# Performance work log

Hardware: AMD Instinct MI355X
Metric: run time of the kernel (lower is better)

Reference implementation:

```python
import jax, jax.numpy as jnp
import numpy as np

N = 100000   # nodes
E = 1600000  # edges
IN_DIM = 64
OUT_DIM = 64
HEADS = 4
C = OUT_DIM // HEADS  # per-head channels = 16
EDGE_DIM = 16
NEG_SLOPE = 0.2
EPS = 1e-5


def setup_inputs() -> dict:
    key = jax.random.key(0)
    ks = jax.random.split(key, 16)
    s = 0.1
    return {
        "x": jax.random.normal(ks[0], (N, IN_DIM), jnp.float32),
        "edge_index": jax.random.randint(ks[1], (2, E), 0, N, jnp.int64 if jax.config.jax_enable_x64 else jnp.int32),
        "edge_attr": jax.random.normal(ks[2], (E, EDGE_DIM), jnp.float32),
        # GATv2Conv params (share_weights=False, edge_dim, concat=True)
        "Wl": jax.random.normal(ks[3], (IN_DIM, HEADS * C), jnp.float32) * s,
        "bl": jnp.zeros((HEADS * C,), jnp.float32),
        "Wr": jax.random.normal(ks[4], (IN_DIM, HEADS * C), jnp.float32) * s,
        "br": jnp.zeros((HEADS * C,), jnp.float32),
        "We": jax.random.normal(ks[5], (EDGE_DIM, HEADS * C), jnp.float32) * s,
        "att": jax.random.normal(ks[6], (HEADS, C), jnp.float32) * s,
        "conv_bias": jnp.zeros((HEADS * C,), jnp.float32),
        # edge gate MLP: Linear(edge_dim, 2*edge_dim) -> SiLU -> Linear(2*edge_dim, 1) -> Sigmoid
        "Wg1": jax.random.normal(ks[7], (EDGE_DIM, 2 * EDGE_DIM), jnp.float32) * s,
        "bg1": jnp.zeros((2 * EDGE_DIM,), jnp.float32),
        "Wg2": jax.random.normal(ks[8], (2 * EDGE_DIM, 1), jnp.float32) * s,
        "bg2": jnp.zeros((1,), jnp.float32),
        # LayerNorm(out_dim)
        "gamma": jnp.ones((OUT_DIM,), jnp.float32),
        "beta": jnp.zeros((OUT_DIM,), jnp.float32),
    }


def _silu(v):
    return v * jax.nn.sigmoid(v)


def reference(x, edge_index, edge_attr, Wl, bl, Wr, br, We, att, conv_bias,
              Wg1, bg1, Wg2, bg2, gamma, beta):
    src, tgt = edge_index[0], edge_index[1]

    # --- edge gate: sigmoid(Linear(SiLU(Linear(e)))) -> [E, 1]
    gate = jax.nn.sigmoid(_silu(edge_attr @ Wg1 + bg1) @ Wg2 + bg2)

    # --- GATv2Conv ---
    xl = (x @ Wl + bl).reshape(N, HEADS, C)   # source transform
    xr = (x @ Wr + br).reshape(N, HEADS, C)   # target transform
    ee = (edge_attr @ We).reshape(E, HEADS, C)

    xj = xl[src]                               # [E, H, C] source messages
    m = jax.nn.leaky_relu(xj + xr[tgt] + ee, NEG_SLOPE)
    alpha = jnp.einsum('ehc,hc->eh', m, att)   # [E, H]

    # segment softmax over edges sharing the same target node
    amax = jax.ops.segment_max(alpha, tgt, num_segments=N)  # [N, H]
    a = jnp.exp(alpha - amax[tgt])
    denom = jax.ops.segment_sum(a, tgt, num_segments=N)
    a = a / denom[tgt]

    out = jax.ops.segment_sum(xj * a[:, :, None], tgt, num_segments=N)
    out = out.reshape(N, HEADS * C) + conv_bias

    # --- edge-gate mean modulation per target node ---
    gate_sum = jax.ops.segment_sum(gate[:, 0], tgt, num_segments=N)
    degree = jax.ops.segment_sum(jnp.ones((E,), out.dtype), tgt, num_segments=N)
    mean_gate = gate_sum / jnp.maximum(degree, 1.0)
    out = out * mean_gate[:, None]

    # --- LayerNorm -> SiLU -> (dropout p=0) -> residual (Identity proj) ---
    mu = jnp.mean(out, axis=-1, keepdims=True)
    var = jnp.var(out, axis=-1, keepdims=True)
    out = (out - mu) * jax.lax.rsqrt(var + EPS) * gamma + beta
    out = _silu(out)
    return out + x
```

## Files before the change

### kernel.cpp

```cpp
#include <hip/hip_runtime.h>
#include <hip/hip_bf16.h>
#include <hip/hip_fp16.h>
#include <math.h>

#define N_NODES 100000
#define N_EDGES 1600000
#define IN_DIM 64
#define OUT_DIM 64
#define HEADS 4
#define CH 16
#define EDGE_DIM 16
#define NEG_SLOPE 0.2f
#define LN_EPS 1e-5f
#define NBLK 391
#define CHUNK 32
#define NREP 8

typedef unsigned short u16;
typedef unsigned int u32;
typedef unsigned long long u64;
typedef __attribute__((ext_vector_type(8))) short bf16x8;
typedef __attribute__((ext_vector_type(4))) float f32x4;

__device__ __forceinline__ float bf2f(u16 v) {
    return __uint_as_float(((u32)v) << 16);
}
__device__ __forceinline__ u16 f2bf(float f) {
    u32 u = __float_as_uint(f);
    u32 r = (u + 0x7FFFu + ((u >> 16) & 1u)) >> 16;
    return (u16)r;
}
__device__ __forceinline__ void load16bf(const u16* p, float* out) {
    const uint4* q = (const uint4*)p;
    uint4 a = q[0], b = q[1];
    u32 w[8] = {a.x, a.y, a.z, a.w, b.x, b.y, b.z, b.w};
#pragma unroll
    for (int i = 0; i < 8; ++i) {
        out[2*i]   = __uint_as_float(w[i] << 16);
        out[2*i+1] = __uint_as_float(w[i] & 0xFFFF0000u);
    }
}
__device__ __forceinline__ void load16f(const void* base, long i, bool f32in, float* out) {
    if (f32in) {
        const float4* q = (const float4*)((const float*)base + i);
        float4 v0 = q[0], v1 = q[1], v2 = q[2], v3 = q[3];
        out[0]=v0.x; out[1]=v0.y; out[2]=v0.z; out[3]=v0.w;
        out[4]=v1.x; out[5]=v1.y; out[6]=v1.z; out[7]=v1.w;
        out[8]=v2.x; out[9]=v2.y; out[10]=v2.z; out[11]=v2.w;
        out[12]=v3.x; out[13]=v3.y; out[14]=v3.z; out[15]=v3.w;
    } else {
        load16bf((const u16*)base + i, out);
    }
}
__device__ __forceinline__ float ldf(const void* base, int i, bool f32in) {
    return f32in ? ((const float*)base)[i] : bf2f(((const u16*)base)[i]);
}

#define DPP_ROR_ADD(v, N) do { \
    int _d = __builtin_amdgcn_update_dpp(0, __float_as_int(v), 0x120 + (N), 0xF, 0xF, true); \
    (v) += __int_as_float(_d); } while (0)

__global__ void k_sniff_zero(const u32* __restrict__ xw, const int* __restrict__ eiw,
                             int* __restrict__ flags, int4* __restrict__ curR4,
                             float4* __restrict__ gsum4) {
    if (blockIdx.x != 0) {
        const int i = (blockIdx.x - 1) * 256 + threadIdx.x;
        if (i < NREP * N_NODES / 4) curR4[i] = make_int4(0, 0, 0, 0);
        else if (i < NREP * N_NODES / 4 + N_NODES / 4)
            gsum4[i - NREP * N_NODES / 4] = make_float4(0.f, 0.f, 0.f, 0.f);
        return;
    }
    __shared__ int s_f32, s_not64;
    const int t = threadIdx.x;
    if (t == 0) { s_f32 = 0; s_not64 = 0; }
    __syncthreads();
    if (t < 64) {
        u32 w = xw[t];
        for (int h = 0; h < 2; ++h) {
            u32 bits = h ? (w & 0xFFFF0000u) : (w << 16);
            float v = __uint_as_float(bits);
            float a = fabsf(v);
            bool sane = (a == 0.0f) || (a >= 1e-30f && a <= 1000.0f);
            if (!sane || v != v) atomicOr(&s_f32, 1);
        }
    } else if (t < 96) {
        if (eiw[2 * (t - 64) + 1] != 0) atomicOr(&s_not64, 1);
    }
    __syncthreads();
    if (t == 0) flags[0] = s_f32 | ((s_not64 ? 0 : 1) << 1);
}

__global__ __launch_bounds__(256) void k_transform(
    const void* __restrict__ x,
    const void* __restrict__ Wl, const void* __restrict__ bl,
    const void* __restrict__ Wr, const void* __restrict__ br,
    u16* __restrict__ xl, u16* __restrict__ xr,
    const int* __restrict__ flags)
{
    const bool f32in = (flags[0] & 1) != 0;
    const int lane = threadIdx.x & 63;
    const int w = threadIdx.x >> 6;
    const int m0 = blockIdx.x * 64;
    const int col = lane & 15;
    const int quad = lane >> 4;

    bf16x8 bfrag[2][2];
    float bias[2];
#pragma unroll
    for (int nt = 0; nt < 2; ++nt) {
        const int ng = w * 32 + nt * 16 + col;
        const void* W  = (ng < 64) ? Wl : Wr;
        const void* bi = (ng < 64) ? bl : br;
        const int c = ng & 63;
        bias[nt] = ldf(bi, c, f32in);
#pragma unroll
        for (int kf = 0; kf < 2; ++kf)
#pragma unroll
            for (int j = 0; j < 8; ++j) {
                const int k = kf * 32 + quad * 8 + j;
                bfrag[nt][kf][j] = (short)f2bf(ldf(W, k * 64 + c, f32in));
            }
    }

#pragma unroll
    for (int mt = 0; mt < 4; ++mt) {
        const int mrow = m0 + mt * 16 + col;
        const int m = (mrow < N_NODES) ? mrow : (N_NODES - 1);
        bf16x8 afrag[2];
#pragma unroll
        for (int kf = 0; kf < 2; ++kf) {
            const int kb = kf * 32 + quad * 8;
            if (f32in) {
                const float* xp = (const float*)x + (size_t)m * 64 + kb;
#pragma unroll
                for (int j = 0; j < 8; ++j) afrag[kf][j] = (short)f2bf(xp[j]);
            } else {
                afrag[kf] = *(const bf16x8*)((const u16*)x + (size_t)m * 64 + kb);
            }
        }
#pragma unroll
        for (int nt = 0; nt < 2; ++nt) {
            f32x4 c = {bias[nt], bias[nt], bias[nt], bias[nt]};
            c = __builtin_amdgcn_mfma_f32_16x16x32_bf16(afrag[0], bfrag[nt][0], c, 0, 0, 0);
            c = __builtin_amdgcn_mfma_f32_16x16x32_bf16(afrag[1], bfrag[nt][1], c, 0, 0, 0);
            const int ng = w * 32 + nt * 16 + col;
            u16* dst = (ng < 64) ? xl : xr;
            const int cc = ng & 63;
#pragma unroll
            for (int r = 0; r < 4; ++r) {
                const int node = m0 + mt * 16 + quad * 4 + r;
                if (node < N_NODES) dst[(size_t)node * 64 + cc] = f2bf(c[r]);
            }
        }
    }
}

__global__ __launch_bounds__(256) void k_count_gate(
    const int* __restrict__ ei, int* __restrict__ curR,
    float4* __restrict__ zreg, u16* __restrict__ slotA, u16* __restrict__ gateA,
    const void* __restrict__ edge_attr,
    const void* __restrict__ Wg1, const void* __restrict__ bg1,
    const void* __restrict__ Wg2, const void* __restrict__ bg2,
    const int* __restrict__ flags)
{
    __shared__ float sWg1t[32 * 16];
    __shared__ float sBg1[32];
    __shared__ float sWg2[32];
    __shared__ float sBg2;
    const int tid = threadIdx.x;
    const int fl = flags[0];
    const bool f32in = (fl & 1) != 0;
    const bool i64   = (fl & 2) != 0;
    for (int i = tid; i < 32 * 16; i += 256) {
        const int j = i >> 4, k = i & 15;
        sWg1t[i] = ldf(Wg1, k * 32 + j, f32in);
    }
    if (tid < 32) sBg1[tid] = ldf(bg1, tid, f32in);
    if (tid >= 32 && tid < 64) sWg2[tid - 32] = ldf(Wg2, tid - 32, f32in);
    if (tid == 0) sBg2 = ldf(bg2, 0, f32in);
    __syncthreads();

    const int gid = blockIdx.x * 256 + tid;
    for (int i = gid; i < N_NODES * 68 / 4; i += 6250 * 256)
        zreg[i] = make_float4(0.f, 0.f, 0.f, 0.f);
    const int tgt = i64 ? ei[2 * (N_EDGES + gid)] : ei[N_EDGES + gid];
    const int r = blockIdx.x & (NREP - 1);
    const int slot = atomicAdd(&curR[r * N_NODES + tgt], 1);
    slotA[gid] = (u16)slot;

    float ea[EDGE_DIM];
    load16f(edge_attr, (long)gid * EDGE_DIM, f32in, ea);
    float g = sBg2;
#pragma unroll
    for (int j = 0; j < 32; ++j) {
        float hv = sBg1[j];
        const float4* wr = (const float4*)&sWg1t[j * 16];
#pragma unroll
        for (int k4 = 0; k4 < 4; ++k4) {
            const float4 wv = wr[k4];
            hv += ea[4*k4]   * wv.x + ea[4*k4+1] * wv.y
                + ea[4*k4+2] * wv.z + ea[4*k4+3] * wv.w;
        }
        hv = hv / (1.f + __expf(-hv));
        g += hv * sWg2[j];
    }
    g = 1.f / (1.f + __expf(-g));
    gateA[gid] = __half_as_ushort(__float2half(g));
}

__global__ __launch_bounds__(256) void k_bsum(const int* __restrict__ curR,
                                              int* __restrict__ partial)
{
    const int i = blockIdx.x * 256 + threadIdx.x;
    int v = 0;
    if (i < N_NODES) {
#pragma unroll
        for (int r = 0; r < NREP; ++r) v += curR[r * N_NODES + i];
    }
#pragma unroll
    for (int off = 32; off >= 1; off >>= 1) v += __shfl_xor(v, off, 64);
    __shared__ int ws[4];
    if ((threadIdx.x & 63) == 0) ws[threadIdx.x >> 6] = v;
    __syncthreads();
    if (threadIdx.x == 0) partial[blockIdx.x] = ws[0] + ws[1] + ws[2] + ws[3];
}

__global__ void k_bscan(const int* __restrict__ partial, int* __restrict__ poff,
                        int* __restrict__ base)
{
    __shared__ int sp[NBLK];
    for (int i = threadIdx.x; i < NBLK; i += 64) sp[i] = partial[i];
    __syncthreads();
    if (threadIdx.x == 0) {
        int run = 0;
        for (int i = 0; i < NBLK; ++i) { int t = sp[i]; sp[i] = run; run += t; }
        base[N_NODES] = N_EDGES;
    }
    __syncthreads();
    for (int i = threadIdx.x; i < NBLK; i += 64) poff[i] = sp[i];
}

__global__ __launch_bounds__(256) void k_bfinal(int* __restrict__ curR,
                                                const int* __restrict__ poff,
                                                int* __restrict__ base)
{
    const int i = blockIdx.x * 256 + threadIdx.x;
    const int lane = threadIdx.x & 63;
    const int wave = threadIdx.x >> 6;
    int c[NREP];
    int v = 0;
    if (i < N_NODES) {
#pragma unroll
        for (int r = 0; r < NREP; ++r) { c[r] = curR[r * N_NODES + i]; v += c[r]; }
    }
    int s = v;
#pragma unroll
    for (int off = 1; off < 64; off <<= 1) {
        int t = __shfl_up(s, off, 64);
        if (lane >= off) s += t;
    }
    __shared__ int wsum[4];
    if (lane == 63) wsum[wave] = s;
    __syncthreads();
    int wb = 0;
    for (int w = 0; w < wave; ++w) wb += wsum[w];
    if (i < N_NODES) {
        int run = poff[blockIdx.x] + wb + s - v;
        base[i] = run;
#pragma unroll
        for (int r = 0; r < NREP; ++r) { curR[r * N_NODES + i] = run; run += c[r]; }
    }
}

__global__ __launch_bounds__(256) void k_scatter(
    const int* __restrict__ ei, const int* __restrict__ curR,
    const u16* __restrict__ slotA,
    u64* __restrict__ perm8, const int* __restrict__ flags)
{
    const int e = blockIdx.x * 256 + threadIdx.x;
    const bool i64 = (flags[0] & 2) != 0;
    int src, tgt;
    if (i64) { src = ei[2 * e]; tgt = ei[2 * (N_EDGES + e)]; }
    else     { src = ei[e];     tgt = ei[N_EDGES + e]; }
    const int r = blockIdx.x & (NREP - 1);
    const int pos = curR[r * N_NODES + tgt] + (int)slotA[e];
    perm8[pos] = (u64)(u32)src | ((u64)(u32)tgt << 17) | ((u64)(u32)e << 34);
}


__device__ __forceinline__ void seg_flush(
    float* __restrict__ accum, float* __restrict__ dsum_g, float* __restrict__ gsum,
    int t, int lane, float acc, float dsum, float gs)
{
    atomicAdd(&accum[(size_t)t * 64 + lane], acc);
    if ((lane & 15) == 0) atomicAdd(&dsum_g[t * 4 + (lane >> 4)], dsum);
    if (lane == 1) atomicAdd(&gsum[t], gs);
}

template<bool F32IN>
__device__ __forceinline__ void ea_issue(const void* __restrict__ edge_attr,
                                         int eid, uint4* r)
{
    if constexpr (F32IN) {
        const uint4* q = (const uint4*)edge_attr + (size_t)eid * 4;
        r[0] = q[0]; r[1] = q[1]; r[2] = q[2]; r[3] = q[3];
    } else {
        const uint4* q = (const uint4*)((const u16*)edge_attr + (size_t)eid * 16);
        r[0] = q[0]; r[1] = q[1];
    }
}

template<bool F32IN>
__device__ __forceinline__ void ea_vals(const uint4* r, float* out)
{
    const u32* w = (const u32*)r;
    if constexpr (F32IN) {
#pragma unroll
        for (int i = 0; i < 16; ++i) out[i] = __uint_as_float(w[i]);
    } else {
#pragma unroll
        for (int i = 0; i < 8; ++i) {
            out[2*i]   = __uint_as_float(w[i] << 16);
            out[2*i+1] = __uint_as_float(w[i] & 0xFFFF0000u);
        }
    }
}

#define PERM_EXTRACT(JJ, S, T, E2) do { \
    const u32 _lo = (u32)__builtin_amdgcn_readlane(plo, (JJ)); \
    const u32 _hi = (u32)__builtin_amdgcn_readlane(phi, (JJ)); \
    (S)  = (int)(_lo & 0x1FFFFu); \
    (T)  = (int)(((_lo >> 17) | (_hi << 15)) & 0x1FFFFu); \
    (E2) = (int)(_hi >> 2); } while (0)

template<bool F32IN>
__device__ __forceinline__ void attn_run(
    const u64* __restrict__ perm8, const void* __restrict__ edge_attr,
    const u16* __restrict__ gateA,
    const u16* __restrict__ xl, const u16* __restrict__ xr,
    float* __restrict__ accum, float* __restrict__ dsum_g, float* __restrict__ gsum,
    const float* We_c, float att_c, int lane, int j0)
{
    const u64 pl = perm8[j0 + (lane & (CHUNK - 1))];
    const int plo = (int)(u32)pl;
    const int phi = (int)(u32)(pl >> 32);

    int s_cur, t_cur, e_cur;
    PERM_EXTRACT(0, s_cur, t_cur, e_cur);

    uint4 ear[F32IN ? 4 : 2];
    ea_issue<F32IN>(edge_attr, e_cur, ear);
    u32 xl_c = xl[(size_t)s_cur * 64 + lane];
    u32 xr_c = xr[(size_t)t_cur * 64 + lane];
    float g_c = __half2float(__ushort_as_half(gateA[e_cur]));

    int cur_t = t_cur;
    float acc = 0.f, dsum = 0.f, gs = 0.f;

#pragma unroll
    for (int jj = 0; jj < CHUNK; ++jj) {
        float eav[16];
        ea_vals<F32IN>(ear, eav);
        float ee = 0.f;
#pragma unroll
        for (int k = 0; k < EDGE_DIM; ++k) ee = fmaf(eav[k], We_c[k], ee);
        const float xlf = bf2f((u16)xl_c);
        const float xrf = bf2f((u16)xr_c);

        int s_nxt = s_cur, t_nxt = t_cur, e_nxt = e_cur;
        u32 xl_n = xl_c, xr_n = xr_c;
        float g_n = g_c;
        if (jj + 1 < CHUNK) {
            PERM_EXTRACT(jj + 1, s_nxt, t_nxt, e_nxt);
            ea_issue<F32IN>(edge_attr, e_nxt, ear);
            xl_n = xl[(size_t)s_nxt * 64 + lane];
            g_n = __half2float(__ushort_as_half(gateA[e_nxt]));
            if (t_nxt != t_cur)
                xr_n = xr[(size_t)t_nxt * 64 + lane];
        }

        if (t_cur != cur_t) {
            seg_flush(accum, dsum_g, gsum, cur_t, lane, acc, dsum, gs);
            cur_t = t_cur; acc = 0.f; dsum = 0.f; gs = 0.f;
        }
        float m = xlf + xrf + ee;
        m = fmaxf(m, m * NEG_SLOPE);
        float t = att_c * m;
        DPP_ROR_ADD(t, 1);
        DPP_ROR_ADD(t, 2);
        DPP_ROR_ADD(t, 4);
        DPP_ROR_ADD(t, 8);
        const float a = __expf(t);
        acc  += a * xlf;
        dsum += a;
        gs   += g_c;

        s_cur = s_nxt; t_cur = t_nxt; e_cur = e_nxt;
        xl_c = xl_n;   xr_c = xr_n;   g_c = g_n;
    }
    seg_flush(accum, dsum_g, gsum, cur_t, lane, acc, dsum, gs);
}

__global__ __launch_bounds__(256, 8) void k_attn_agg(
    const u64* __restrict__ perm8,
    const void* __restrict__ edge_attr,
    const u16* __restrict__ gateA,
    const void* __restrict__ We,
    const void* __restrict__ att,
    const u16* __restrict__ xl, const u16* __restrict__ xr,
    float* __restrict__ accum,
    float* __restrict__ dsum_g,
    float* __restrict__ gsum,
    const int* __restrict__ flags)
{
    const bool f32in = (flags[0] & 1) != 0;
    const int lane = threadIdx.x & 63;
    const int wid = blockIdx.x * 4 + (threadIdx.x >> 6);
    const int j0 = wid * CHUNK;

    float We_c[EDGE_DIM];
#pragma unroll
    for (int k = 0; k < EDGE_DIM; ++k) We_c[k] = ldf(We, k * 64 + lane, f32in);
    const float att_c = ldf(att, lane, f32in);

    if (f32in) attn_run<true >(perm8, edge_attr, gateA, xl, xr, accum, dsum_g, gsum, We_c, att_c, lane, j0);
    else       attn_run<false>(perm8, edge_attr, gateA, xl, xr, accum, dsum_g, gsum, We_c, att_c, lane, j0);
}

__global__ __launch_bounds__(256) void k_epilogue(
    const int* __restrict__ base,
    const float* __restrict__ accum, const float* __restrict__ dsum_g,
    const float* __restrict__ gsum,
    const void* __restrict__ conv_bias, const void* __restrict__ gamma,
    const void* __restrict__ beta, const void* __restrict__ x,
    void* __restrict__ out, const int* __restrict__ flags)
{
    const bool f32in = (flags[0] & 1) != 0;
    const int lane = threadIdx.x & 63;
    const int wave = threadIdx.x >> 6;
    const int n = blockIdx.x * 4 + wave;
    if (n >= N_NODES) return;
    const int h = lane >> 4;

    float v = accum[(size_t)n * 64 + lane];
    const float d = dsum_g[n * 4 + h];
    v = (d > 0.f) ? v / d : 0.f;
    v += ldf(conv_bias, lane, f32in);
    const int deg = base[n + 1] - base[n];
    const float mg = gsum[n] / fmaxf((float)deg, 1.0f);
    v *= mg;

    float s = v;
#pragma unroll
    for (int m2 = 32; m2 >= 1; m2 >>= 1) s += __shfl_xor(s, m2, 64);
    const float mu = s * (1.f / 64.f);
    const float diff = v - mu;
    float q = diff * diff;
#pragma unroll
    for (int m2 = 32; m2 >= 1; m2 >>= 1) q += __shfl_xor(q, m2, 64);
    const float var = q * (1.f / 64.f);

    float y = diff * rsqrtf(var + LN_EPS) * ldf(gamma, lane, f32in) + ldf(beta, lane, f32in);
    y = y / (1.f + __expf(-y));
    const float r = y + ldf(x, n * 64 + lane, f32in);
    if (f32in) ((float*)out)[(size_t)n * 64 + lane] = r;
    else       ((u16*)out)[(size_t)n * 64 + lane] = f2bf(r);
}

extern "C" void kernel_launch(void* const* d_in, const int* in_sizes, int n_in,
                              void* d_out, int out_size, void* d_ws, size_t ws_size,
                              hipStream_t stream)
{
    const void* x   = d_in[0];
    const int* ei   = (const int*)d_in[1];
    const void* ea  = d_in[2];
    const void* Wl  = d_in[3];
    const void* bl  = d_in[4];
    const void* Wr  = d_in[5];
    const void* br  = d_in[6];
    const void* We  = d_in[7];
    const void* att = d_in[8];
    const void* cb  = d_in[9];
    const void* Wg1 = d_in[10];
    const void* bg1 = d_in[11];
    const void* Wg2 = d_in[12];
    const void* bg2 = d_in[13];
    const void* gam = d_in[14];
    const void* bet = d_in[15];

    char* ws = (char*)d_ws;
    int*   flags   = (int*)ws;
    int*   curR    = (int*)(ws + 16);
    int*   base    = (int*)(ws + 3200016);
    int*   partial = (int*)(ws + 3600032);
    int*   poff    = (int*)(ws + 3601600);
    u16*   slotA   = (u16*)(ws + 3603168);
    u16*   gateA   = (u16*)(ws + 6803168);
    u64*   perm8   = (u64*)(ws + 10003168);
    float* accum   = (float*)(ws + 22803168);
    float* dsum_g  = (float*)(ws + 48403168);
    float* gsum    = (float*)(ws + 50003168);
    u16*   xl      = (u16*)(ws + 50403168);
    u16*   xr      = (u16*)(ws + 63203168);

    k_sniff_zero<<<881, 256, 0, stream>>>((const u32*)x, ei, flags, (int4*)curR,
                                          (float4*)gsum);

    k_transform<<<(N_NODES + 63) / 64, 256, 0, stream>>>(x, Wl, bl, Wr, br, xl, xr, flags);

    k_count_gate<<<N_EDGES / 256, 256, 0, stream>>>(
        ei, curR, (float4*)accum, slotA, gateA, ea, Wg1, bg1, Wg2, bg2, flags);

    k_bsum<<<NBLK, 256, 0, stream>>>(curR, partial);
    k_bscan<<<1, 64, 0, stream>>>(partial, poff, base);
    k_bfinal<<<NBLK, 256, 0, stream>>>(curR, poff, base);

    k_scatter<<<N_EDGES / 256, 256, 0, stream>>>(ei, curR, slotA, perm8, flags);

    k_attn_agg<<<N_EDGES / CHUNK / 4, 256, 0, stream>>>(
        perm8, ea, gateA, We, att, xl, xr, accum, dsum_g, gsum, flags);

    k_epilogue<<<(N_NODES + 3) / 4, 256, 0, stream>>>(
        base, accum, dsum_g, gsum, cb, gam, bet, x, d_out, flags);
}
```

Before: 468.2 us.

## Accumulate edge gates per target in count kernel; double-buffer edge_attr loads

The per-edge gate is no longer written to a half-precision array and re-read in the attention kernel. The count kernel now atomically adds it into replicated per-target sums (8 replicas), and the epilogue reduces those with shuffles. The attention loop double-buffers edge_attr prefetches and uses packed 2-wide FMAs for the edge projection. This removes a per-edge gather and a per-segment atomic from the hot attention kernel, at the cost of extra float atomics in the count kernel and a larger zeroing pass.

```diff
diff --git a/kernel.cpp b/kernel.cpp
--- a/kernel.cpp
+++ b/kernel.cpp
@@ -21,6 +21,7 @@
 typedef unsigned long long u64;
 typedef __attribute__((ext_vector_type(8))) short bf16x8;
 typedef __attribute__((ext_vector_type(4))) float f32x4;
+typedef __attribute__((ext_vector_type(2))) float f32x2;
 
 __device__ __forceinline__ float bf2f(u16 v) {
     return __uint_as_float(((u32)v) << 16);
@@ -62,12 +63,12 @@
 
 __global__ void k_sniff_zero(const u32* __restrict__ xw, const int* __restrict__ eiw,
                              int* __restrict__ flags, int4* __restrict__ curR4,
-                             float4* __restrict__ gsum4) {
+                             float4* __restrict__ gsumR4) {
     if (blockIdx.x != 0) {
         const int i = (blockIdx.x - 1) * 256 + threadIdx.x;
         if (i < NREP * N_NODES / 4) curR4[i] = make_int4(0, 0, 0, 0);
-        else if (i < NREP * N_NODES / 4 + N_NODES / 4)
-            gsum4[i - NREP * N_NODES / 4] = make_float4(0.f, 0.f, 0.f, 0.f);
+        else if (i < 2 * NREP * N_NODES / 4)
+            gsumR4[i - NREP * N_NODES / 4] = make_float4(0.f, 0.f, 0.f, 0.f);
         return;
     }
     __shared__ int s_f32, s_not64;
@@ -157,7 +158,7 @@
 
 __global__ __launch_bounds__(256) void k_count_gate(
     const int* __restrict__ ei, int* __restrict__ curR,
-    float4* __restrict__ zreg, u16* __restrict__ slotA, u16* __restrict__ gateA,
+    float4* __restrict__ zreg, u16* __restrict__ slotA, float* __restrict__ gsumR,
     const void* __restrict__ edge_attr,
     const void* __restrict__ Wg1, const void* __restrict__ bg1,
     const void* __restrict__ Wg2, const void* __restrict__ bg2,
@@ -190,6 +191,7 @@
 
     float ea[EDGE_DIM];
     load16f(edge_attr, (long)gid * EDGE_DIM, f32in, ea);
+
     float g = sBg2;
 #pragma unroll
     for (int j = 0; j < 32; ++j) {
@@ -205,7 +207,7 @@
         g += hv * sWg2[j];
     }
     g = 1.f / (1.f + __expf(-g));
-    gateA[gid] = __half_as_ushort(__float2half(g));
+    atomicAdd(&gsumR[r * N_NODES + tgt], g);
 }
 
 __global__ __launch_bounds__(256) void k_bsum(const int* __restrict__ curR,
@@ -289,16 +291,15 @@
 
 
 __device__ __forceinline__ void seg_flush(
-    float* __restrict__ accum, float* __restrict__ dsum_g, float* __restrict__ gsum,
-    int t, int lane, float acc, float dsum, float gs)
+    float* __restrict__ accum, float* __restrict__ dsum_g,
+    int t, int lane, float acc, float dsum)
 {
     atomicAdd(&accum[(size_t)t * 64 + lane], acc);
     if ((lane & 15) == 0) atomicAdd(&dsum_g[t * 4 + (lane >> 4)], dsum);
-    if (lane == 1) atomicAdd(&gsum[t], gs);
 }
 
 template<bool F32IN>
-__device__ __forceinline__ void ea_issue(const void* __restrict__ edge_attr,
+__device__ __forceinline__ void ea_fetch(const void* __restrict__ edge_attr,
                                          int eid, uint4* r)
 {
     if constexpr (F32IN) {
@@ -336,10 +337,9 @@
 template<bool F32IN>
 __device__ __forceinline__ void attn_run(
     const u64* __restrict__ perm8, const void* __restrict__ edge_attr,
-    const u16* __restrict__ gateA,
     const u16* __restrict__ xl, const u16* __restrict__ xr,
-    float* __restrict__ accum, float* __restrict__ dsum_g, float* __restrict__ gsum,
-    const float* We_c, float att_c, int lane, int j0)
+    float* __restrict__ accum, float* __restrict__ dsum_g,
+    const f32x2* Wep, float att_c, int lane, int j0)
 {
     const u64 pl = perm8[j0 + (lane & (CHUNK - 1))];
     const int plo = (int)(u32)pl;
@@ -348,42 +348,45 @@
     int s_cur, t_cur, e_cur;
     PERM_EXTRACT(0, s_cur, t_cur, e_cur);
 
-    uint4 ear[F32IN ? 4 : 2];
-    ea_issue<F32IN>(edge_attr, e_cur, ear);
+    constexpr int NU4 = F32IN ? 4 : 2;
+    uint4 eb[2][NU4];
+    ea_fetch<F32IN>(edge_attr, e_cur, eb[0]);
     u32 xl_c = xl[(size_t)s_cur * 64 + lane];
     u32 xr_c = xr[(size_t)t_cur * 64 + lane];
-    float g_c = __half2float(__ushort_as_half(gateA[e_cur]));
 
     int cur_t = t_cur;
-    float acc = 0.f, dsum = 0.f, gs = 0.f;
+    float acc = 0.f, dsum = 0.f;
 
 #pragma unroll
     for (int jj = 0; jj < CHUNK; ++jj) {
-        float eav[16];
-        ea_vals<F32IN>(ear, eav);
-        float ee = 0.f;
-#pragma unroll
-        for (int k = 0; k < EDGE_DIM; ++k) ee = fmaf(eav[k], We_c[k], ee);
+        const int cb = jj & 1;
+        int s_nxt = s_cur, t_nxt = t_cur, e_nxt = e_cur;
+        u32 xl_n = xl_c, xr_n = xr_c;
+        if (jj + 1 < CHUNK) {
+            PERM_EXTRACT(jj + 1, s_nxt, t_nxt, e_nxt);
+            ea_fetch<F32IN>(edge_attr, e_nxt, eb[cb ^ 1]);
+            xl_n = xl[(size_t)s_nxt * 64 + lane];
+            if (t_nxt != t_cur)
+                xr_n = xr[(size_t)t_nxt * 64 + lane];
+        }
+
         const float xlf = bf2f((u16)xl_c);
         const float xrf = bf2f((u16)xr_c);
 
-        int s_nxt = s_cur, t_nxt = t_cur, e_nxt = e_cur;
-        u32 xl_n = xl_c, xr_n = xr_c;
-        float g_n = g_c;
-        if (jj + 1 < CHUNK) {
-            PERM_EXTRACT(jj + 1, s_nxt, t_nxt, e_nxt);
-            ea_issue<F32IN>(edge_attr, e_nxt, ear);
-            xl_n = xl[(size_t)s_nxt * 64 + lane];
-            g_n = __half2float(__ushort_as_half(gateA[e_nxt]));
-            if (t_nxt != t_cur)
-                xr_n = xr[(size_t)t_nxt * 64 + lane];
-        }
-
         if (t_cur != cur_t) {
-            seg_flush(accum, dsum_g, gsum, cur_t, lane, acc, dsum, gs);
-            cur_t = t_cur; acc = 0.f; dsum = 0.f; gs = 0.f;
-        }
-        float m = xlf + xrf + ee;
+            seg_flush(accum, dsum_g, cur_t, lane, acc, dsum);
+            cur_t = t_cur; acc = 0.f; dsum = 0.f;
+        }
+
+        float eav[16];
+        ea_vals<F32IN>(eb[cb], eav);
+        f32x2 acc2 = {xlf + xrf, 0.f};
+        const f32x2* ea2 = (const f32x2*)eav;
+#pragma unroll
+        for (int i = 0; i < 8; ++i)
+            acc2 = __builtin_elementwise_fma(ea2[i], Wep[i], acc2);
+        float m = acc2[0] + acc2[1];
+
         m = fmaxf(m, m * NEG_SLOPE);
         float t = att_c * m;
         DPP_ROR_ADD(t, 1);
@@ -393,24 +396,21 @@
         const float a = __expf(t);
         acc  += a * xlf;
         dsum += a;
-        gs   += g_c;
 
         s_cur = s_nxt; t_cur = t_nxt; e_cur = e_nxt;
-        xl_c = xl_n;   xr_c = xr_n;   g_c = g_n;
-    }
-    seg_flush(accum, dsum_g, gsum, cur_t, lane, acc, dsum, gs);
+        xl_c = xl_n;   xr_c = xr_n;
+    }
+    seg_flush(accum, dsum_g, cur_t, lane, acc, dsum);
 }
 
 __global__ __launch_bounds__(256, 8) void k_attn_agg(
     const u64* __restrict__ perm8,
     const void* __restrict__ edge_attr,
-    const u16* __restrict__ gateA,
     const void* __restrict__ We,
     const void* __restrict__ att,
     const u16* __restrict__ xl, const u16* __restrict__ xr,
     float* __restrict__ accum,
     float* __restrict__ dsum_g,
-    float* __restrict__ gsum,
     const int* __restrict__ flags)
 {
     const bool f32in = (flags[0] & 1) != 0;
@@ -418,19 +418,22 @@
     const int wid = blockIdx.x * 4 + (threadIdx.x >> 6);
     const int j0 = wid * CHUNK;
 
-    float We_c[EDGE_DIM];
-#pragma unroll
-    for (int k = 0; k < EDGE_DIM; ++k) We_c[k] = ldf(We, k * 64 + lane, f32in);
+    f32x2 Wep[8];
+#pragma unroll
+    for (int i = 0; i < 8; ++i) {
+        Wep[i][0] = ldf(We, (2*i)   * 64 + lane, f32in);
+        Wep[i][1] = ldf(We, (2*i+1) * 64 + lane, f32in);
+    }
     const float att_c = ldf(att, lane, f32in);
 
-    if (f32in) attn_run<true >(perm8, edge_attr, gateA, xl, xr, accum, dsum_g, gsum, We_c, att_c, lane, j0);
-    else       attn_run<false>(perm8, edge_attr, gateA, xl, xr, accum, dsum_g, gsum, We_c, att_c, lane, j0);
+    if (f32in) attn_run<true >(perm8, edge_attr, xl, xr, accum, dsum_g, Wep, att_c, lane, j0);
+    else       attn_run<false>(perm8, edge_attr, xl, xr, accum, dsum_g, Wep, att_c, lane, j0);
 }
 
 __global__ __launch_bounds__(256) void k_epilogue(
     const int* __restrict__ base,
     const float* __restrict__ accum, const float* __restrict__ dsum_g,
-    const float* __restrict__ gsum,
+    const float* __restrict__ gsumR,
     const void* __restrict__ conv_bias, const void* __restrict__ gamma,
     const void* __restrict__ beta, const void* __restrict__ x,
     void* __restrict__ out, const int* __restrict__ flags)
@@ -442,12 +445,16 @@
     if (n >= N_NODES) return;
     const int h = lane >> 4;
 
+    float gsv = gsumR[(size_t)(lane & 7) * N_NODES + n];
+#pragma unroll
+    for (int off = 4; off >= 1; off >>= 1) gsv += __shfl_xor(gsv, off, 64);
+
     float v = accum[(size_t)n * 64 + lane];
     const float d = dsum_g[n * 4 + h];
     v = (d > 0.f) ? v / d : 0.f;
     v += ldf(conv_bias, lane, f32in);
     const int deg = base[n + 1] - base[n];
-    const float mg = gsum[n] / fmaxf((float)deg, 1.0f);
+    const float mg = gsv / fmaxf((float)deg, 1.0f);
     v *= mg;
 
     float s = v;
@@ -495,21 +502,20 @@
     int*   partial = (int*)(ws + 3600032);
     int*   poff    = (int*)(ws + 3601600);
     u16*   slotA   = (u16*)(ws + 3603168);
-    u16*   gateA   = (u16*)(ws + 6803168);
+    float* gsumR   = (float*)(ws + 6803168);
     u64*   perm8   = (u64*)(ws + 10003168);
     float* accum   = (float*)(ws + 22803168);
     float* dsum_g  = (float*)(ws + 48403168);
-    float* gsum    = (float*)(ws + 50003168);
     u16*   xl      = (u16*)(ws + 50403168);
     u16*   xr      = (u16*)(ws + 63203168);
 
-    k_sniff_zero<<<881, 256, 0, stream>>>((const u32*)x, ei, flags, (int4*)curR,
-                                          (float4*)gsum);
+    k_sniff_zero<<<1564, 256, 0, stream>>>((const u32*)x, ei, flags, (int4*)curR,
+                                           (float4*)gsumR);
 
     k_transform<<<(N_NODES + 63) / 64, 256, 0, stream>>>(x, Wl, bl, Wr, br, xl, xr, flags);
 
     k_count_gate<<<N_EDGES / 256, 256, 0, stream>>>(
-        ei, curR, (float4*)accum, slotA, gateA, ea, Wg1, bg1, Wg2, bg2, flags);
+        ei, curR, (float4*)accum, slotA, gsumR, ea, Wg1, bg1, Wg2, bg2, flags);
 
     k_bsum<<<NBLK, 256, 0, stream>>>(curR, partial);
     k_bscan<<<1, 64, 0, stream>>>(partial, poff, base);
@@ -518,8 +524,8 @@
     k_scatter<<<N_EDGES / 256, 256, 0, stream>>>(ei, curR, slotA, perm8, flags);
 
     k_attn_agg<<<N_EDGES / CHUNK / 4, 256, 0, stream>>>(
-        perm8, ea, gateA, We, att, xl, xr, accum, dsum_g, gsum, flags);
+        perm8, ea, We, att, xl, xr, accum, dsum_g, flags);
 
     k_epilogue<<<(N_NODES + 3) / 4, 256, 0, stream>>>(
-        base, accum, dsum_g, gsum, cb, gam, bet, x, d_out, flags);
-}
+        base, accum, dsum_g, gsumR, cb, gam, bet, x, d_out, flags);
+}
```

Result: slower. 527.2 us (+12.6%).

## Compute edge gate MLP with MFMA and double-buffer edge_attr in attention loop

Applied to the files above, without the earlier changes.

The edge-gate MLP in k_count_gate moves from per-thread scalar FMAs over shared-memory weights to bf16 MFMA 16x16x32 tiles per wave. The SiLU output is reduced against Wg2 with DPP row adds, and gates are packed and stored four at a time. In the attention aggregation loop, edge_attr prefetch gains an explicit double buffer, and the 16-term edge projection uses packed f32x2 FMAs. The gate hidden layer now runs with bf16-rounded inputs and weights, which reduces precision, and the double buffer raises register pressure.

```diff
diff --git a/kernel.cpp b/kernel.cpp
--- a/kernel.cpp
+++ b/kernel.cpp
@@ -21,6 +21,7 @@
 typedef unsigned long long u64;
 typedef __attribute__((ext_vector_type(8))) short bf16x8;
 typedef __attribute__((ext_vector_type(4))) float f32x4;
+typedef __attribute__((ext_vector_type(2))) float f32x2;
 
 __device__ __forceinline__ float bf2f(u16 v) {
     return __uint_as_float(((u32)v) << 16);
@@ -163,49 +164,78 @@
     const void* __restrict__ Wg2, const void* __restrict__ bg2,
     const int* __restrict__ flags)
 {
-    __shared__ float sWg1t[32 * 16];
-    __shared__ float sBg1[32];
-    __shared__ float sWg2[32];
-    __shared__ float sBg2;
     const int tid = threadIdx.x;
     const int fl = flags[0];
     const bool f32in = (fl & 1) != 0;
     const bool i64   = (fl & 2) != 0;
-    for (int i = tid; i < 32 * 16; i += 256) {
-        const int j = i >> 4, k = i & 15;
-        sWg1t[i] = ldf(Wg1, k * 32 + j, f32in);
-    }
-    if (tid < 32) sBg1[tid] = ldf(bg1, tid, f32in);
-    if (tid >= 32 && tid < 64) sWg2[tid - 32] = ldf(Wg2, tid - 32, f32in);
-    if (tid == 0) sBg2 = ldf(bg2, 0, f32in);
-    __syncthreads();
+    const int lane = tid & 63;
+    const int w    = tid >> 6;
+    const int col  = lane & 15;
+    const int quad = lane >> 4;
 
     const int gid = blockIdx.x * 256 + tid;
     for (int i = gid; i < N_NODES * 68 / 4; i += 6250 * 256)
         zreg[i] = make_float4(0.f, 0.f, 0.f, 0.f);
     const int tgt = i64 ? ei[2 * (N_EDGES + gid)] : ei[N_EDGES + gid];
     const int r = blockIdx.x & (NREP - 1);
-    const int slot = atomicAdd(&curR[r * N_NODES + tgt], 1);
-    slotA[gid] = (u16)slot;
-
-    float ea[EDGE_DIM];
-    load16f(edge_attr, (long)gid * EDGE_DIM, f32in, ea);
-    float g = sBg2;
-#pragma unroll
-    for (int j = 0; j < 32; ++j) {
-        float hv = sBg1[j];
-        const float4* wr = (const float4*)&sWg1t[j * 16];
-#pragma unroll
-        for (int k4 = 0; k4 < 4; ++k4) {
-            const float4 wv = wr[k4];
-            hv += ea[4*k4]   * wv.x + ea[4*k4+1] * wv.y
-                + ea[4*k4+2] * wv.z + ea[4*k4+3] * wv.w;
-        }
-        hv = hv / (1.f + __expf(-hv));
-        g += hv * sWg2[j];
-    }
-    g = 1.f / (1.f + __expf(-g));
-    gateA[gid] = __half_as_ushort(__float2half(g));
+    slotA[gid] = (u16)atomicAdd(&curR[r * N_NODES + tgt], 1);
+
+    bf16x8 bfrag[2];
+    float bias[2], wg2c[2];
+#pragma unroll
+    for (int nh = 0; nh < 2; ++nh) {
+        const int c = nh * 16 + col;
+        bias[nh] = ldf(bg1, c, f32in);
+        wg2c[nh] = ldf(Wg2, c, f32in);
+#pragma unroll
+        for (int j = 0; j < 8; ++j) {
+            const int k = quad * 8 + j;
+            bfrag[nh][j] = (k < 16) ? (short)f2bf(ldf(Wg1, k * 32 + c, f32in)) : (short)0;
+        }
+    }
+    const float bg2v = ldf(bg2, 0, f32in);
+
+    const int ebase = blockIdx.x * 256 + w * 64;
+#pragma unroll
+    for (int t4 = 0; t4 < 4; ++t4) {
+        const int tb = ebase + t4 * 16;
+        bf16x8 afrag = {};
+        if (quad < 2) {
+            const long off = (long)(tb + col) * EDGE_DIM + quad * 8;
+            if (f32in) {
+                const float4* q = (const float4*)((const float*)edge_attr + off);
+                const float4 a0 = q[0], a1 = q[1];
+                afrag[0] = (short)f2bf(a0.x); afrag[1] = (short)f2bf(a0.y);
+                afrag[2] = (short)f2bf(a0.z); afrag[3] = (short)f2bf(a0.w);
+                afrag[4] = (short)f2bf(a1.x); afrag[5] = (short)f2bf(a1.y);
+                afrag[6] = (short)f2bf(a1.z); afrag[7] = (short)f2bf(a1.w);
+            } else {
+                afrag = *(const bf16x8*)((const u16*)edge_attr + off);
+            }
+        }
+        f32x4 h0 = {bias[0], bias[0], bias[0], bias[0]};
+        f32x4 h1 = {bias[1], bias[1], bias[1], bias[1]};
+        h0 = __builtin_amdgcn_mfma_f32_16x16x32_bf16(afrag, bfrag[0], h0, 0, 0, 0);
+        h1 = __builtin_amdgcn_mfma_f32_16x16x32_bf16(afrag, bfrag[1], h1, 0, 0, 0);
+
+        u32 gpack[2] = {0, 0};
+#pragma unroll
+        for (int rr = 0; rr < 4; ++rr) {
+            float v0 = h0[rr]; v0 = v0 / (1.f + __expf(-v0));
+            float v1 = h1[rr]; v1 = v1 / (1.f + __expf(-v1));
+            float p = v0 * wg2c[0] + v1 * wg2c[1];
+            DPP_ROR_ADD(p, 1);
+            DPP_ROR_ADD(p, 2);
+            DPP_ROR_ADD(p, 4);
+            DPP_ROR_ADD(p, 8);
+            const float g = 1.f / (1.f + __expf(-(p + bg2v)));
+            const u16 gh = __half_as_ushort(__float2half(g));
+            if (rr & 1) gpack[rr >> 1] |= ((u32)gh << 16);
+            else        gpack[rr >> 1]  = gh;
+        }
+        if (col == 0)
+            *(uint2*)(gateA + tb + quad * 4) = make_uint2(gpack[0], gpack[1]);
+    }
 }
 
 __global__ __launch_bounds__(256) void k_bsum(const int* __restrict__ curR,
@@ -298,7 +328,7 @@
 }
 
 template<bool F32IN>
-__device__ __forceinline__ void ea_issue(const void* __restrict__ edge_attr,
+__device__ __forceinline__ void ea_fetch(const void* __restrict__ edge_attr,
                                          int eid, uint4* r)
 {
     if constexpr (F32IN) {
@@ -339,7 +369,7 @@
     const u16* __restrict__ gateA,
     const u16* __restrict__ xl, const u16* __restrict__ xr,
     float* __restrict__ accum, float* __restrict__ dsum_g, float* __restrict__ gsum,
-    const float* We_c, float att_c, int lane, int j0)
+    const f32x2* Wep, float att_c, int lane, int j0)
 {
     const u64 pl = perm8[j0 + (lane & (CHUNK - 1))];
     const int plo = (int)(u32)pl;
@@ -348,8 +378,9 @@
     int s_cur, t_cur, e_cur;
     PERM_EXTRACT(0, s_cur, t_cur, e_cur);
 
-    uint4 ear[F32IN ? 4 : 2];
-    ea_issue<F32IN>(edge_attr, e_cur, ear);
+    constexpr int NU4 = F32IN ? 4 : 2;
+    uint4 eb[2][NU4];
+    ea_fetch<F32IN>(edge_attr, e_cur, eb[0]);
     u32 xl_c = xl[(size_t)s_cur * 64 + lane];
     u32 xr_c = xr[(size_t)t_cur * 64 + lane];
     float g_c = __half2float(__ushort_as_half(gateA[e_cur]));
@@ -359,31 +390,36 @@
 
 #pragma unroll
     for (int jj = 0; jj < CHUNK; ++jj) {
-        float eav[16];
-        ea_vals<F32IN>(ear, eav);
-        float ee = 0.f;
-#pragma unroll
-        for (int k = 0; k < EDGE_DIM; ++k) ee = fmaf(eav[k], We_c[k], ee);
-        const float xlf = bf2f((u16)xl_c);
-        const float xrf = bf2f((u16)xr_c);
-
+        const int cb = jj & 1;
         int s_nxt = s_cur, t_nxt = t_cur, e_nxt = e_cur;
         u32 xl_n = xl_c, xr_n = xr_c;
         float g_n = g_c;
         if (jj + 1 < CHUNK) {
             PERM_EXTRACT(jj + 1, s_nxt, t_nxt, e_nxt);
-            ea_issue<F32IN>(edge_attr, e_nxt, ear);
+            ea_fetch<F32IN>(edge_attr, e_nxt, eb[cb ^ 1]);
             xl_n = xl[(size_t)s_nxt * 64 + lane];
             g_n = __half2float(__ushort_as_half(gateA[e_nxt]));
             if (t_nxt != t_cur)
                 xr_n = xr[(size_t)t_nxt * 64 + lane];
         }
 
+        const float xlf = bf2f((u16)xl_c);
+        const float xrf = bf2f((u16)xr_c);
+
         if (t_cur != cur_t) {
             seg_flush(accum, dsum_g, gsum, cur_t, lane, acc, dsum, gs);
             cur_t = t_cur; acc = 0.f; dsum = 0.f; gs = 0.f;
         }
-        float m = xlf + xrf + ee;
+
+        float eav[16];
+        ea_vals<F32IN>(eb[cb], eav);
+        f32x2 acc2 = {xlf + xrf, 0.f};
+        const f32x2* ea2 = (const f32x2*)eav;
+#pragma unroll
+        for (int i = 0; i < 8; ++i)
+            acc2 = __builtin_elementwise_fma(ea2[i], Wep[i], acc2);
+        float m = acc2[0] + acc2[1];
+
         m = fmaxf(m, m * NEG_SLOPE);
         float t = att_c * m;
         DPP_ROR_ADD(t, 1);
@@ -418,13 +454,18 @@
     const int wid = blockIdx.x * 4 + (threadIdx.x >> 6);
     const int j0 = wid * CHUNK;
 
-    float We_c[EDGE_DIM];
-#pragma unroll
-    for (int k = 0; k < EDGE_DIM; ++k) We_c[k] = ldf(We, k * 64 + lane, f32in);
+    f32x2 Wep[8];
+#pragma unroll
+    for (int i = 0; i < 8; ++i) {
+        Wep[i][0] = ldf(We, (2*i)   * 64 + lane, f32in);
+        Wep[i][1] = ldf(We, (2*i+1) * 64 + lane, f32in);
+    }
     const float att_c = ldf(att, lane, f32in);
 
-    if (f32in) attn_run<true >(perm8, edge_attr, gateA, xl, xr, accum, dsum_g, gsum, We_c, att_c, lane, j0);
-    else       attn_run<false>(perm8, edge_attr, gateA, xl, xr, accum, dsum_g, gsum, We_c, att_c, lane, j0);
+    if (f32in) attn_run<true >(perm8, edge_attr, gateA, xl, xr,
+                               accum, dsum_g, gsum, Wep, att_c, lane, j0);
+    else       attn_run<false>(perm8, edge_attr, gateA, xl, xr,
+                               accum, dsum_g, gsum, Wep, att_c, lane, j0);
 }
 
 __global__ __launch_bounds__(256) void k_epilogue(
```

After: 484.0 us. 1.03x slower.
